# Kernel optimization log

Measured on AMD Instinct MI355X. Metric: run time of the kernel, lower is better.

The kernel has to match this reference:

```python
import jax, jax.numpy as jnp
import numpy as np

B, T, D_IN, D_H, D_CODE, N_CODES, D_OUT = 64, 512, 1024, 512, 256, 128, 100


def setup_inputs() -> dict:
    key = jax.random.key(0)
    ks = jax.random.split(key, 8)
    x = jax.random.normal(ks[0], (B, T, D_IN), dtype=jnp.float32)
    W1 = jax.random.normal(ks[1], (D_IN, D_H), dtype=jnp.float32) * (1.0 / np.sqrt(D_IN))
    b1 = jnp.zeros((D_H,), jnp.float32)
    W2 = jax.random.normal(ks[2], (D_H, D_CODE), dtype=jnp.float32) * (1.0 / np.sqrt(D_H))
    b2 = jnp.zeros((D_CODE,), jnp.float32)
    codebook = jax.random.normal(ks[3], (N_CODES, D_CODE), dtype=jnp.float32)
    Wd = jax.random.normal(ks[4], (D_CODE, D_OUT), dtype=jnp.float32) * (1.0 / np.sqrt(D_CODE))
    bd = jnp.zeros((D_OUT,), jnp.float32)
    return {"x": x, "W1": W1, "b1": b1, "W2": W2, "b2": b2,
            "codebook": codebook, "Wd": Wd, "bd": bd}


def reference(x, W1, b1, W2, b2, codebook, Wd, bd):
    Bb, Tt, _ = x.shape
    # Encoder (per-timestep loop in torch == one batched matmul)
    h = jax.nn.relu(jnp.einsum('btd,dh->bth', x, W1) + b1)
    encoded = jnp.einsum('bth,hc->btc', h, W2) + b2          # [B,T,256]
    flat = encoded.reshape(-1, D_CODE)                        # [B*T,256]
    # Squared euclidean distances (argmin identical to cdist argmin)
    d2 = (jnp.sum(flat * flat, axis=1, keepdims=True)
          - 2.0 * flat @ codebook.T
          + jnp.sum(codebook * codebook, axis=1))             # [B*T,128]
    token_indices = jnp.argmin(d2, axis=-1)                   # [B*T]
    quantized = codebook[token_indices].reshape(Bb, Tt, D_CODE)
    commitment_loss = jnp.mean((encoded - jax.lax.stop_gradient(quantized)) ** 2)
    codebook_loss = jnp.mean((quantized - jax.lax.stop_gradient(encoded)) ** 2)
    # decoded is computed in the torch model but never returned (dead code)
    pooled = encoded.mean(axis=1)
    decoded = pooled @ Wd + bd  # noqa: F841 (pruned by XLA, kept for fidelity)
    total_loss = commitment_loss + 0.25 * codebook_loss
    return (token_indices.reshape(Bb, Tt), commitment_loss, codebook_loss, total_loss)
```

## Files before the change

### kernel.cpp

```cpp
#include <hip/hip_runtime.h>
#include <cstddef>
#include <cstdint>

static constexpr int M_ROWS  = 32768;
static constexpr int D_INK   = 1024;
static constexpr int D_HID   = 512;
static constexpr int D_CODE_ = 256;
static constexpr int N_CODES_= 128;

static constexpr float TAU_GAP = 0.15f;

using f16x8 = __attribute__((ext_vector_type(8))) _Float16;
using f32x4 = __attribute__((ext_vector_type(4))) float;

__device__ __forceinline__ float rdlane(float v, int kk) {
    return __uint_as_float(__builtin_amdgcn_readlane(__float_as_uint(v), kk));
}


__device__ __forceinline__ void dma16(const void* g, void* l) {
    __builtin_amdgcn_global_load_lds(
        (const __attribute__((address_space(1))) void*)g,
        (__attribute__((address_space(3))) void*)l, 16, 0, 0);
}

__device__ __forceinline__ void stage_panel(const _Float16* __restrict__ p,
                                            _Float16* dst, int w, int lane)
{
    #pragma unroll
    for (int ii = 0; ii < 2; ++ii) {
        const int I = 2 * w + ii;
        dma16(p + (size_t)I * 512 + lane * 8, dst + (size_t)I * 512);
    }
}

__device__ __forceinline__ void mfma_tile(const _Float16* sA, const _Float16* sB,
                                          int wm, int wn, int kq, int lm,
                                          f32x4 (&acc)[4][4])
{
    f16x8 a[4];
    #pragma unroll
    for (int fm = 0; fm < 4; ++fm)
        a[fm] = *(const f16x8*)(sA + (kq * 128 + wm * 64 + fm * 16 + lm) * 8);
    #pragma unroll
    for (int fn = 0; fn < 4; ++fn) {
        const f16x8 b = *(const f16x8*)(sB + (kq * 128 + wn * 64 + fn * 16 + lm) * 8);
        #pragma unroll
        for (int fm = 0; fm < 4; ++fm)
            acc[fm][fn] = __builtin_amdgcn_mfma_f32_16x16x32_f16(a[fm], b, acc[fm][fn], 0, 0, 0);
    }
}

__device__ __forceinline__ int xcd_swz(int bid, int nwg) {
    const int q = nwg >> 3;
    return (bid & 7) * q + (bid >> 3);
}

__global__ __launch_bounds__(256)
void prep_cb_kernel(const float* __restrict__ cb, _Float16* __restrict__ cbP,
                    float* __restrict__ cbT,
                    float* __restrict__ cbnorm, float* __restrict__ accum,
                    int* __restrict__ cnt)
{
    const int j = blockIdx.x;
    const int t = threadIdx.x;
    const float v = cb[j * D_CODE_ + t];
    const int ks = t >> 5, kq = (t >> 3) & 3, jj = t & 7;
    cbP[((size_t)ks * 512 + kq * 128 + j) * 8 + jj] = (_Float16)v;
    cbT[(size_t)t * N_CODES_ + j] = v;

    __shared__ float sr[256];
    sr[t] = v * v;
    __syncthreads();
    for (int s = 128; s >= 1; s >>= 1) {
        if (t < s) sr[t] += sr[t + s];
        __syncthreads();
    }
    if (t == 0) cbnorm[j] = sr[0];
    if (j == 0 && t < 2) accum[t] = 0.0f;
    if (j == 0 && t == 2) *cnt = 0;
}

__global__ __launch_bounds__(256)
void pack_w_kernel(const float* __restrict__ W, _Float16* __restrict__ WP,
                   int Kd, int Nd)
{
    const int ks = blockIdx.x, nt = blockIdx.y;
    const int t = threadIdx.x;
    _Float16* dst = WP + ((size_t)nt * (Kd >> 5) + ks) * 4096;
    #pragma unroll
    for (int half = 0; half < 2; ++half) {
        const int f = half * 256 + t;
        const int nc = f & 127, kq = f >> 7;
        f16x8 v;
        #pragma unroll
        for (int j = 0; j < 8; ++j)
            v[j] = (_Float16)W[(size_t)(ks * 32 + kq * 8 + j) * Nd + nt * 128 + nc];
        *(f16x8*)(dst + (size_t)f * 8) = v;
    }
}

__global__ __launch_bounds__(256)
void pack_x_kernel(const float* __restrict__ X, _Float16* __restrict__ XP)
{
    __shared__ _Float16 sh[128][136];
    const int t  = threadIdx.x;
    const int mt = blockIdx.x;
    const int kc = blockIdx.y;

    const float* src = X + (size_t)mt * 128 * D_INK + kc * 128;
    #pragma unroll
    for (int i = 0; i < 16; ++i) {
        const int idx = i * 256 + t;
        const int row = idx >> 5, c4 = idx & 31;
        const float4 v = *(const float4*)(src + (size_t)row * D_INK + c4 * 4);
        _Float16* d = &sh[row][c4 * 4];
        d[0] = (_Float16)v.x; d[1] = (_Float16)v.y;
        d[2] = (_Float16)v.z; d[3] = (_Float16)v.w;
    }
    __syncthreads();

    _Float16* dst = XP + ((size_t)mt * 32 + kc * 4) * 4096;
    #pragma unroll
    for (int s = 0; s < 4; ++s) {
        #pragma unroll
        for (int half = 0; half < 2; ++half) {
            const int f = half * 256 + t;
            const int rc = f & 127, kq = f >> 7;
            const f16x8 v = *(const f16x8*)(&sh[rc][s * 32 + kq * 8]);
            *(f16x8*)(dst + (size_t)s * 4096 + (size_t)f * 8) = v;
        }
    }
}

__global__ __launch_bounds__(256, 4)
void gemm1_kernel(const _Float16* __restrict__ AP, const _Float16* __restrict__ BP,
                  const float* __restrict__ bias, _Float16* __restrict__ CP)
{
    __shared__ _Float16 lds[2][2][4096];

    const int tid  = threadIdx.x;
    const int lane = tid & 63;
    const int w    = tid >> 6;
    const int wm = w >> 1, wn = w & 1;
    const int kq = lane >> 4, lm = lane & 15;

    const int swz = xcd_swz(blockIdx.x, (M_ROWS / 128) * (D_HID / 128));
    const int n0 = (swz & 3) * 128;
    const int m0 = (swz >> 2) * 128;

    const _Float16* Apan = AP + ((size_t)(m0 >> 7) * 32) * 4096;
    const _Float16* Bpan = BP + ((size_t)(n0 >> 7) * 32) * 4096;

    f32x4 acc[4][4] = {};

    stage_panel(Apan, &lds[0][0][0], w, lane);
    stage_panel(Bpan, &lds[0][1][0], w, lane);

    constexpr int NSTEP = D_INK / 32;
    for (int t = 0; t < NSTEP; ++t) {
        const int cur = t & 1, nxt = cur ^ 1;
        __syncthreads();
        if (t + 1 < NSTEP) {
            stage_panel(Apan + (size_t)(t + 1) * 4096, &lds[nxt][0][0], w, lane);
            stage_panel(Bpan + (size_t)(t + 1) * 4096, &lds[nxt][1][0], w, lane);
        }
        mfma_tile(&lds[cur][0][0], &lds[cur][1][0], wm, wn, kq, lm, acc);
    }

    #pragma unroll
    for (int fn = 0; fn < 4; ++fn) {
        const int col = n0 + wn * 64 + fn * 16 + lm;
        const float bv = bias[col];
        #pragma unroll
        for (int fm = 0; fm < 4; ++fm) {
            #pragma unroll
            for (int r = 0; r < 4; ++r) {
                const int row = m0 + wm * 64 + fm * 16 + kq * 4 + r;
                const float v = fmaxf(acc[fm][fn][r] + bv, 0.0f);
                CP[(((size_t)(row >> 7) * 16 + (col >> 5)) * 512
                    + (size_t)((col >> 3) & 3) * 128 + (row & 127)) * 8 + (col & 7)]
                    = (_Float16)v;
            }
        }
    }
}

__global__ __launch_bounds__(256, 4)
void gemm2_kernel(const _Float16* __restrict__ AP, const _Float16* __restrict__ BP,
                  const float* __restrict__ bias, _Float16* __restrict__ CP,
                  float* __restrict__ accum)
{
    __shared__ _Float16 lds[2][2][4096];

    const int tid  = threadIdx.x;
    const int lane = tid & 63;
    const int w    = tid >> 6;
    const int wm = w >> 1, wn = w & 1;
    const int kq = lane >> 4, lm = lane & 15;

    const int swz = xcd_swz(blockIdx.x, (M_ROWS / 128) * (D_CODE_ / 128));
    const int n0 = (swz & 1) * 128;
    const int m0 = (swz >> 1) * 128;

    const _Float16* Apan = AP + ((size_t)(m0 >> 7) * 16) * 4096;
    const _Float16* Bpan = BP + ((size_t)(n0 >> 7) * 16) * 4096;

    f32x4 acc[4][4] = {};

    stage_panel(Apan, &lds[0][0][0], w, lane);
    stage_panel(Bpan, &lds[0][1][0], w, lane);

    constexpr int NSTEP = D_HID / 32;
    for (int t = 0; t < NSTEP; ++t) {
        const int cur = t & 1, nxt = cur ^ 1;
        __syncthreads();
        if (t + 1 < NSTEP) {
            stage_panel(Apan + (size_t)(t + 1) * 4096, &lds[nxt][0][0], w, lane);
            stage_panel(Bpan + (size_t)(t + 1) * 4096, &lds[nxt][1][0], w, lane);
        }
        mfma_tile(&lds[cur][0][0], &lds[cur][1][0], wm, wn, kq, lm, acc);
    }

    float sumsq = 0.0f;
    #pragma unroll
    for (int fn = 0; fn < 4; ++fn) {
        const int col = n0 + wn * 64 + fn * 16 + lm;
        const float bv = bias[col];
        #pragma unroll
        for (int fm = 0; fm < 4; ++fm) {
            #pragma unroll
            for (int r = 0; r < 4; ++r) {
                const int row = m0 + wm * 64 + fm * 16 + kq * 4 + r;
                const float v = acc[fm][fn][r] + bv;
                sumsq = fmaf(v, v, sumsq);
                CP[(((size_t)(row >> 7) * 8 + (col >> 5)) * 512
                    + (size_t)((col >> 3) & 3) * 128 + (row & 127)) * 8 + (col & 7)]
                    = (_Float16)v;
            }
        }
    }
    #pragma unroll
    for (int mk = 1; mk <= 32; mk <<= 1) sumsq += __shfl_xor(sumsq, mk);
    if (lane == 0) atomicAdd(&accum[1], sumsq);
}

__global__ __launch_bounds__(256, 4)
void dist_kernel(const _Float16* __restrict__ AP, const _Float16* __restrict__ BP,
                 const float* __restrict__ cbn,
                 float* __restrict__ outIdx, float* __restrict__ accum,
                 int* __restrict__ cnt, int* __restrict__ list)
{
    __shared__ _Float16 lds[2][2][4096];

    const int tid  = threadIdx.x;
    const int lane = tid & 63;
    const int w    = tid >> 6;
    const int wm = w >> 1, wn = w & 1;
    const int kq = lane >> 4, lm = lane & 15;
    const int m0 = blockIdx.x * 128;

    float cbn_l[4];
    #pragma unroll
    for (int fn = 0; fn < 4; ++fn) cbn_l[fn] = cbn[wn * 64 + fn * 16 + lm];

    const _Float16* Apan = AP + ((size_t)(m0 >> 7) * 8) * 4096;

    f32x4 acc[4][4] = {};

    stage_panel(Apan, &lds[0][0][0], w, lane);
    stage_panel(BP,   &lds[0][1][0], w, lane);

    constexpr int NSTEP = D_CODE_ / 32;
    for (int t = 0; t < NSTEP; ++t) {
        const int cur = t & 1, nxt = cur ^ 1;
        __syncthreads();
        if (t + 1 < NSTEP) {
            stage_panel(Apan + (size_t)(t + 1) * 4096, &lds[nxt][0][0], w, lane);
            stage_panel(BP   + (size_t)(t + 1) * 4096, &lds[nxt][1][0], w, lane);
        }
        mfma_tile(&lds[cur][0][0], &lds[cur][1][0], wm, wn, kq, lm, acc);
    }

    __syncthreads();
    float* eb1 = (float*)&lds[0][0][0];
    float* eb2 = eb1 + 256;
    int*   eix = (int*)(eb2 + 256);

    #pragma unroll
    for (int fm = 0; fm < 4; ++fm) {
        #pragma unroll
        for (int r = 0; r < 4; ++r) {
            float b1v = 3.4e38f, b2v = 3.4e38f; int bi = 0;
            #pragma unroll
            for (int fn = 0; fn < 4; ++fn) {
                const float v = fmaf(-2.0f, acc[fm][fn][r], cbn_l[fn]);
                if (v < b1v) { b2v = b1v; b1v = v; bi = wn * 64 + fn * 16 + lm; }
                else if (v < b2v) b2v = v;
            }
            #pragma unroll
            for (int mk = 1; mk <= 8; mk <<= 1) {
                const float o1 = __shfl_xor(b1v, mk);
                const float o2 = __shfl_xor(b2v, mk);
                const int   oi = __shfl_xor(bi,  mk);
                if (o1 < b1v || (o1 == b1v && oi < bi)) { b2v = fminf(b1v, o2); b1v = o1; bi = oi; }
                else b2v = fminf(b2v, o1);
            }
            const int rl = wm * 64 + fm * 16 + kq * 4 + r;
            if (lm == 0) { eb1[wn * 128 + rl] = b1v; eb2[wn * 128 + rl] = b2v; eix[wn * 128 + rl] = bi; }
        }
    }
    __syncthreads();

    if (tid < 128) {
        const int rl = tid;
        const float a1 = eb1[rl], a2 = eb2[rl]; const int ai = eix[rl];
        const float o1 = eb1[128 + rl], o2 = eb2[128 + rl]; const int oi = eix[128 + rl];
        float B1, B2; int BI;
        if (o1 < a1 || (o1 == a1 && oi < ai)) { B1 = o1; BI = oi; B2 = fminf(a1, o2); }
        else                                  { B1 = a1; BI = ai; B2 = fminf(a2, o1); }
        outIdx[m0 + rl] = (float)BI;
        if (B2 - B1 < TAU_GAP) { const int p = atomicAdd(cnt, 1); list[p] = m0 + rl; }
        float s = B1;
        #pragma unroll
        for (int mk = 1; mk <= 32; mk <<= 1) s += __shfl_xor(s, mk);
        if (lane == 0) atomicAdd(&accum[0], s);
    }
}

__global__ __launch_bounds__(256)
void fixup_kernel(const float* __restrict__ x, const float* __restrict__ W1,
                  const float* __restrict__ b1, const float* __restrict__ W2,
                  const float* __restrict__ b2, const float* __restrict__ cbT,
                  const float* __restrict__ cbnorm,
                  const int* __restrict__ cnt, const int* __restrict__ list,
                  float* __restrict__ outIdx)
{
    __shared__ float xr[8][1024];
    __shared__ float hr[8][512];
    __shared__ float er[8][256];
    __shared__ float dv[8][128];
    __shared__ int   di[8][128];

    const int tid  = threadIdx.x;
    const int lane = tid & 63;
    const int n = *cnt;
    const int ngroups = (n + 7) >> 3;

    for (int g = blockIdx.x; g < ngroups; g += gridDim.x) {
        const int base = g * 8;
        const int nr = n - base < 8 ? n - base : 8;
        __syncthreads();
        #pragma unroll
        for (int r = 0; r < 8; ++r) {
            if (r < nr) {
                const int row = list[base + r];
                *(float4*)&xr[r][tid * 4] =
                    *(const float4*)(x + (size_t)row * D_INK + tid * 4);
            }
        }
        __syncthreads();

        {
            const int c = tid * 2;
            float a0[8], a1[8];
            #pragma unroll
            for (int r = 0; r < 8; ++r) { a0[r] = 0.f; a1[r] = 0.f; }
            for (int k0 = 0; k0 < D_INK; k0 += 64) {
                float xreg[8];
                #pragma unroll
                for (int r = 0; r < 8; ++r) xreg[r] = xr[r][k0 + lane];
                #pragma unroll 8
                for (int kk = 0; kk < 64; ++kk) {
                    const float2 wv = *(const float2*)(W1 + (size_t)(k0 + kk) * D_HID + c);
                    #pragma unroll
                    for (int r = 0; r < 8; ++r) {
                        const float xv = rdlane(xreg[r], kk);
                        a0[r] = fmaf(xv, wv.x, a0[r]);
                        a1[r] = fmaf(xv, wv.y, a1[r]);
                    }
                }
            }
            #pragma unroll
            for (int r = 0; r < 8; ++r) {
                hr[r][c]     = fmaxf(a0[r] + b1[c], 0.f);
                hr[r][c + 1] = fmaxf(a1[r] + b1[c + 1], 0.f);
            }
        }
        __syncthreads();

        {
            float a[8];
            #pragma unroll
            for (int r = 0; r < 8; ++r) a[r] = 0.f;
            for (int k0 = 0; k0 < D_HID; k0 += 64) {
                float hreg[8];
                #pragma unroll
                for (int r = 0; r < 8; ++r) hreg[r] = hr[r][k0 + lane];
                #pragma unroll 8
                for (int kk = 0; kk < 64; ++kk) {
                    const float wv = W2[(size_t)(k0 + kk) * D_CODE_ + tid];
                    #pragma unroll
                    for (int r = 0; r < 8; ++r)
                        a[r] = fmaf(rdlane(hreg[r], kk), wv, a[r]);
                }
            }
            #pragma unroll
            for (int r = 0; r < 8; ++r)
                er[r][tid] = a[r] + b2[tid];
        }
        __syncthreads();

        {
            const int j = tid & 127, half = tid >> 7;
            float e2[4], dt[4];
            #pragma unroll
            for (int q = 0; q < 4; ++q) { e2[q] = 0.f; dt[q] = 0.f; }
            for (int k0 = 0; k0 < D_CODE_; k0 += 64) {
                float ereg[4];
                #pragma unroll
                for (int q = 0; q < 4; ++q) ereg[q] = er[half * 4 + q][k0 + lane];
                #pragma unroll 8
                for (int kk = 0; kk < 64; ++kk) {
                    const float cv = cbT[(size_t)(k0 + kk) * N_CODES_ + j];
                    #pragma unroll
                    for (int q = 0; q < 4; ++q) {
                        const float ev = rdlane(ereg[q], kk);
                        e2[q] = fmaf(ev, ev, e2[q]);
                        dt[q] = fmaf(ev, cv, dt[q]);
                    }
                }
            }
            #pragma unroll
            for (int q = 0; q < 4; ++q) {
                dv[half * 4 + q][j] = (e2[q] - 2.0f * dt[q]) + cbnorm[j];
                di[half * 4 + q][j] = j;
            }
        }
        __syncthreads();

        #pragma unroll
        for (int pass = 0; pass < 2; ++pass) {
            const int r = pass * 4 + (tid >> 6);
            const int i = tid & 63;
            {
                const float a = dv[r][i], b = dv[r][i + 64];
                const int  ib = di[r][i + 64];
                if (b < a) { dv[r][i] = b; di[r][i] = ib; }
            }
            __syncthreads();
            for (int st = 32; st >= 1; st >>= 1) {
                if (i < st) {
                    const float a = dv[r][i], b = dv[r][i + st];
                    const int  ib = di[r][i + st];
                    if (b < a || (b == a && ib < di[r][i])) { dv[r][i] = b; di[r][i] = ib; }
                }
                __syncthreads();
            }
        }
        if (tid < nr) outIdx[list[base + tid]] = (float)di[tid][0];
    }
}

__global__ void finalize_kernel(const float* __restrict__ accum, float* __restrict__ out)
{
    const float inv = 1.0f / (32768.0f * 256.0f);
    const float loss = (accum[0] + accum[1]) * inv;
    out[32768] = loss;
    out[32769] = loss;
    out[32770] = 1.25f * loss;
}

extern "C" void kernel_launch(void* const* d_in, const int* in_sizes, int n_in,
                              void* d_out, int out_size, void* d_ws, size_t ws_size,
                              hipStream_t stream)
{
    (void)in_sizes; (void)n_in; (void)out_size; (void)ws_size;

    const float* x  = (const float*)d_in[0];
    const float* W1 = (const float*)d_in[1];
    const float* b1 = (const float*)d_in[2];
    const float* W2 = (const float*)d_in[3];
    const float* b2 = (const float*)d_in[4];
    const float* cb = (const float*)d_in[5];
    float* out = (float*)d_out;

    char* ws = (char*)d_ws;
    _Float16* W1P  = (_Float16*)(ws + 0);
    _Float16* W2P  = (_Float16*)(ws + 1048576);
    _Float16* cbP  = (_Float16*)(ws + 1310720);
    float*    cbn  = (float*   )(ws + 1376256);
    float*    accum= (float*   )(ws + 1376768);
    int*      cnt  = (int*     )(ws + 1376832);
    int*      list = (int*     )(ws + 1376896);
    float*    cbT  = (float*   )(ws + 1507968);
    _Float16* xP   = (_Float16*)(ws + (size_t)(2u<<20));
    _Float16* encP = (_Float16*)(ws + (size_t)(2u<<20));
    _Float16* hP   = (_Float16*)(ws + (size_t)(2u<<20) + 67108864);

    prep_cb_kernel<<<N_CODES_, 256, 0, stream>>>(cb, cbP, cbT, cbn, accum, cnt);
    pack_w_kernel<<<dim3(D_INK / 32, D_HID / 128), 256, 0, stream>>>(W1, W1P, D_INK, D_HID);
    pack_w_kernel<<<dim3(D_HID / 32, D_CODE_ / 128), 256, 0, stream>>>(W2, W2P, D_HID, D_CODE_);
    pack_x_kernel<<<dim3(M_ROWS / 128, D_INK / 128), 256, 0, stream>>>(x, xP);

    gemm1_kernel<<<(M_ROWS / 128) * (D_HID / 128), 256, 0, stream>>>(xP, W1P, b1, hP);
    gemm2_kernel<<<(M_ROWS / 128) * (D_CODE_ / 128), 256, 0, stream>>>(hP, W2P, b2, encP, accum);
    dist_kernel<<<M_ROWS / 128, 256, 0, stream>>>(encP, cbP, cbn, out, accum, cnt, list);
    fixup_kernel<<<512, 256, 0, stream>>>(x, W1, b1, W2, b2, cbT, cbn, cnt, list, out);
    finalize_kernel<<<1, 1, 0, stream>>>(accum, out);
}
```

Measured before the change: 253.2 us.

## Stage W1 slabs into LDS with double-buffered DMA in fixup kernel

The fixup kernel's first matmul now streams W1 in 8-row slabs into a double-buffered LDS area using global_load_lds DMA. Each lane holds one x element per slab and broadcasts it with readlane, which replaces the full x-row staging in shared memory. The second matmul is remapped to half the rows per thread with paired f32x2 FMAs, and the argmin reduction is reworked into 128-wide passes. The fixup path handles only ambiguous rows, so its share of total time is uncertain, and the per-slab syncthreads add barrier overhead.

```diff
diff --git a/kernel.cpp b/kernel.cpp
--- a/kernel.cpp
+++ b/kernel.cpp
@@ -12,6 +12,7 @@
 
 using f16x8 = __attribute__((ext_vector_type(8))) _Float16;
 using f32x4 = __attribute__((ext_vector_type(4))) float;
+using f32x2 = __attribute__((ext_vector_type(2))) float;
 
 __device__ __forceinline__ float rdlane(float v, int kk) {
     return __uint_as_float(__builtin_amdgcn_readlane(__float_as_uint(v), kk));
@@ -336,7 +337,7 @@
                   const int* __restrict__ cnt, const int* __restrict__ list,
                   float* __restrict__ outIdx)
 {
-    __shared__ float xr[8][1024];
+    __shared__ float w1s[2][8][512];
     __shared__ float hr[8][512];
     __shared__ float er[8][256];
     __shared__ float dv[8][128];
@@ -344,78 +345,94 @@
 
     const int tid  = threadIdx.x;
     const int lane = tid & 63;
+    const int w    = tid >> 6;
     const int n = *cnt;
     const int ngroups = (n + 7) >> 3;
 
     for (int g = blockIdx.x; g < ngroups; g += gridDim.x) {
         const int base = g * 8;
-        const int nr = n - base < 8 ? n - base : 8;
-        __syncthreads();
+        const int nr = (n - base < 8) ? (n - base) : 8;
+        __syncthreads();
+
+        const int rsel = lane >> 3;
+        const int myrow = list[base + (rsel < nr ? rsel : nr - 1)];
+        const float* xrow = x + (size_t)myrow * D_INK;
+
+        const int c2 = tid * 2;
+        f32x2 a01[8] = {};
+
+        #pragma unroll
+        for (int ii = 0; ii < 4; ++ii) {
+            const int off = (w * 4 + ii) * 256;
+            dma16(W1 + off + lane * 4, &w1s[0][0][0] + off);
+        }
+        float xv_c = xrow[lane & 7];
+        float xv_n = 0.0f;
+
+        constexpr int NSLAB = D_INK / 8;
+        for (int s = 0; s < NSLAB; ++s) {
+            const int cur = s & 1;
+            __syncthreads();
+            if (s + 1 < NSLAB) {
+                const size_t k0n = (size_t)(s + 1) * 8;
+                #pragma unroll
+                for (int ii = 0; ii < 4; ++ii) {
+                    const int off = (w * 4 + ii) * 256;
+                    dma16(W1 + k0n * D_HID + off + lane * 4, &w1s[cur ^ 1][0][0] + off);
+                }
+                xv_n = xrow[k0n + (lane & 7)];
+            }
+            #pragma unroll
+            for (int kk = 0; kk < 8; ++kk) {
+                const f32x2 w01 = *(const f32x2*)&w1s[cur][kk][c2];
+                #pragma unroll
+                for (int r = 0; r < 8; ++r) {
+                    const float xb = rdlane(xv_c, r * 8 + kk);
+                    a01[r] = __builtin_elementwise_fma((f32x2){xb, xb}, w01, a01[r]);
+                }
+            }
+            xv_c = xv_n;
+        }
+
         #pragma unroll
         for (int r = 0; r < 8; ++r) {
-            if (r < nr) {
-                const int row = list[base + r];
-                *(float4*)&xr[r][tid * 4] =
-                    *(const float4*)(x + (size_t)row * D_INK + tid * 4);
-            }
+            hr[r][c2]     = fmaxf(a01[r].x + b1[c2], 0.0f);
+            hr[r][c2 + 1] = fmaxf(a01[r].y + b1[c2 + 1], 0.0f);
         }
         __syncthreads();
 
         {
-            const int c = tid * 2;
-            float a0[8], a1[8];
-            #pragma unroll
-            for (int r = 0; r < 8; ++r) { a0[r] = 0.f; a1[r] = 0.f; }
-            for (int k0 = 0; k0 < D_INK; k0 += 64) {
-                float xreg[8];
+            const int cc = (tid & 127) * 2;
+            const int half = tid >> 7;
+            f32x2 a2[4] = {};
+            for (int k0 = 0; k0 < D_HID; k0 += 64) {
+                float hreg[4];
                 #pragma unroll
-                for (int r = 0; r < 8; ++r) xreg[r] = xr[r][k0 + lane];
+                for (int q = 0; q < 4; ++q) hreg[q] = hr[half * 4 + q][k0 + lane];
                 #pragma unroll 8
                 for (int kk = 0; kk < 64; ++kk) {
-                    const float2 wv = *(const float2*)(W1 + (size_t)(k0 + kk) * D_HID + c);
+                    const f32x2 w01 = *(const f32x2*)&W2[(size_t)(k0 + kk) * D_CODE_ + cc];
                     #pragma unroll
-                    for (int r = 0; r < 8; ++r) {
-                        const float xv = rdlane(xreg[r], kk);
-                        a0[r] = fmaf(xv, wv.x, a0[r]);
-                        a1[r] = fmaf(xv, wv.y, a1[r]);
+                    for (int q = 0; q < 4; ++q) {
+                        const float hb = rdlane(hreg[q], kk);
+                        a2[q] = __builtin_elementwise_fma((f32x2){hb, hb}, w01, a2[q]);
                     }
                 }
             }
             #pragma unroll
-            for (int r = 0; r < 8; ++r) {
-                hr[r][c]     = fmaxf(a0[r] + b1[c], 0.f);
-                hr[r][c + 1] = fmaxf(a1[r] + b1[c + 1], 0.f);
+            for (int q = 0; q < 4; ++q) {
+                er[half * 4 + q][cc]     = a2[q].x + b2[cc];
+                er[half * 4 + q][cc + 1] = a2[q].y + b2[cc + 1];
             }
         }
         __syncthreads();
 
         {
-            float a[8];
-            #pragma unroll
-            for (int r = 0; r < 8; ++r) a[r] = 0.f;
-            for (int k0 = 0; k0 < D_HID; k0 += 64) {
-                float hreg[8];
-                #pragma unroll
-                for (int r = 0; r < 8; ++r) hreg[r] = hr[r][k0 + lane];
-                #pragma unroll 8
-                for (int kk = 0; kk < 64; ++kk) {
-                    const float wv = W2[(size_t)(k0 + kk) * D_CODE_ + tid];
-                    #pragma unroll
-                    for (int r = 0; r < 8; ++r)
-                        a[r] = fmaf(rdlane(hreg[r], kk), wv, a[r]);
-                }
-            }
-            #pragma unroll
-            for (int r = 0; r < 8; ++r)
-                er[r][tid] = a[r] + b2[tid];
-        }
-        __syncthreads();
-
-        {
-            const int j = tid & 127, half = tid >> 7;
+            const int j = tid & 127;
+            const int half = tid >> 7;
             float e2[4], dt[4];
             #pragma unroll
-            for (int q = 0; q < 4; ++q) { e2[q] = 0.f; dt[q] = 0.f; }
+            for (int q = 0; q < 4; ++q) { e2[q] = 0.0f; dt[q] = 0.0f; }
             for (int k0 = 0; k0 < D_CODE_; k0 += 64) {
                 float ereg[4];
                 #pragma unroll
@@ -440,16 +457,10 @@
         __syncthreads();
 
         #pragma unroll
-        for (int pass = 0; pass < 2; ++pass) {
-            const int r = pass * 4 + (tid >> 6);
-            const int i = tid & 63;
-            {
-                const float a = dv[r][i], b = dv[r][i + 64];
-                const int  ib = di[r][i + 64];
-                if (b < a) { dv[r][i] = b; di[r][i] = ib; }
-            }
-            __syncthreads();
-            for (int st = 32; st >= 1; st >>= 1) {
+        for (int pass = 0; pass < 4; ++pass) {
+            const int r = pass * 2 + (tid >> 7);
+            const int i = tid & 127;
+            for (int st = 64; st >= 1; st >>= 1) {
                 if (i < st) {
                     const float a = dv[r][i], b = dv[r][i + st];
                     const int  ib = di[r][i + st];
```

Result: slower. 319.2 us (+26.1%).
